# Performance work log

Measured on AMD Instinct MI355X. Metric: run time of the kernel, lower is better.

## Reference

```python
import jax, jax.numpy as jnp
import numpy as np

NUM_USER = 100000
NUM_ITEM = 50000
DIM_E = 128
DIM_FEAT = 256
BATCH = 1024
NUM_NEG = 127
TEMP = 2.0
LR_LAMBDA = 0.5
NUM_SAMPLE = 0.5


def _l2norm(x, eps=1e-12):
    n = jnp.linalg.norm(x, axis=1, keepdims=True)
    return x / jnp.maximum(n, eps)


def setup_inputs() -> dict:
    key = jax.random.key(0)
    ks = jax.random.split(key, 9)
    flat = BATCH * (1 + NUM_NEG)
    user_tensor = jax.random.randint(ks[0], (BATCH, 1 + NUM_NEG), 0, NUM_USER, dtype=jnp.int64 if jax.config.jax_enable_x64 else jnp.int32)
    item_tensor = jax.random.randint(ks[1], (BATCH, 1 + NUM_NEG), NUM_USER, NUM_USER + NUM_ITEM, dtype=user_tensor.dtype)
    rand_index = jax.random.randint(ks[2], (int(flat * NUM_SAMPLE),), 0, flat, dtype=user_tensor.dtype)
    id_embedding = jax.random.normal(ks[3], (NUM_USER + NUM_ITEM, DIM_E), jnp.float32) * 0.02
    v_feat = jax.random.normal(ks[4], (NUM_ITEM, DIM_FEAT), jnp.float32)
    W1 = jax.random.normal(ks[5], (DIM_FEAT, 256), jnp.float32) * (1.0 / np.sqrt(DIM_FEAT))
    b1 = jax.random.normal(ks[6], (256,), jnp.float32) * 0.01
    W2 = jax.random.normal(ks[7], (256, DIM_E), jnp.float32) * (1.0 / 16.0)
    b2 = jax.random.normal(ks[8], (DIM_E,), jnp.float32) * 0.01
    return {"user_tensor": user_tensor, "item_tensor": item_tensor, "rand_index": rand_index,
            "id_embedding": id_embedding, "v_feat": v_feat, "W1": W1, "b1": b1, "W2": W2, "b2": b2}


def _contrastive(anchor, all_t):
    # exp(<a,b>/T) grouped into [B, 1+num_neg]; pos is column 0
    score = jnp.exp(jnp.sum(anchor * all_t, axis=1) / TEMP).reshape(-1, 1 + NUM_NEG)
    pos = score[:, 0]
    tot = jnp.sum(score, axis=1)
    return jnp.mean(-jnp.log(pos / tot))


def reference(user_tensor, item_tensor, rand_index, id_embedding, v_feat, W1, b1, W2, b2):
    # encoder: normalize content feats, 2-layer MLP
    feature = _l2norm(v_feat)
    feature = jax.nn.leaky_relu(feature @ W1 + b1)  # slope 0.01, matches torch default
    feature = feature @ W2 + b2                      # [num_item, dim_E]

    pos_flat = jnp.repeat(item_tensor[:, 0:1], 1 + NUM_NEG, axis=1).reshape(-1)
    u_flat = user_tensor.reshape(-1)
    i_flat = item_tensor.reshape(-1)

    all_item_feat = feature[i_flat - NUM_USER]          # [flat, dim_E]
    user_emb = id_embedding[u_flat]
    pos_emb = id_embedding[pos_flat]
    all_item_emb = id_embedding[i_flat]

    head_feat = _l2norm(all_item_feat)
    head_embed = _l2norm(pos_emb)

    # replace a random half of the item embeddings with content features
    all_item_input = all_item_emb.at[rand_index].set(all_item_feat[rand_index])

    c1 = _contrastive(head_embed, head_feat)
    c2 = _contrastive(user_emb, all_item_input)

    reg_loss = (jnp.mean(jnp.sqrt(jnp.sum(user_emb ** 2, axis=1))) +
                jnp.mean(jnp.sqrt(jnp.sum(all_item_emb ** 2, axis=1)))) / 2

    # graph_generator is None -> graph contrastive loss is 0
    total = c1 * LR_LAMBDA + c2 * (1.0 - LR_LAMBDA)
    return total, reg_loss
```

## Files before the change

kernel.cpp:

```cpp
#include <hip/hip_runtime.h>
#include <math.h>

#define NUSER 100000
#define NITEM 50000
#define NID   (NUSER + NITEM)
#define DIM_E 128
#define DIM_F 256
#define BATCH 1024
#define NCOL 128
#define FLAT (BATCH * NCOL)

typedef __attribute__((ext_vector_type(8))) short bf16x8;
typedef __attribute__((ext_vector_type(4))) short bf16x4;
typedef __attribute__((ext_vector_type(4))) float f32x4;

__device__ __forceinline__ float dot4(float4 a, float4 b) {
    return a.x * b.x + a.y * b.y + a.z * b.z + a.w * b.w;
}

__device__ __forceinline__ short f2bf(float x) {
    unsigned u = __float_as_uint(x);
    unsigned r = (u + 0x7FFFu + ((u >> 16) & 1u)) >> 16;
    return (short)r;
}

__device__ __forceinline__ float bf2f(short s) {
    return __uint_as_float(((unsigned)(unsigned short)s) << 16);
}

__global__ __launch_bounds__(256) void prep0_kernel(const float* __restrict__ W1,
                                                    const float* __restrict__ W2,
                                                    short* __restrict__ w1t,
                                                    short* __restrict__ w2t,
                                                    int* __restrict__ flags) {
    int i = blockIdx.x * 256 + threadIdx.x;
    if (i < FLAT) flags[i] = 0;
    if (i < 256 * 256) {
        int n = i >> 8, k = i & 255;
        w1t[i] = f2bf(W1[(size_t)k * 256 + n]);
    } else if (i < 256 * 256 + 128 * 256) {
        int j = i - 256 * 256;
        int n = j >> 8, k = j & 255;
        w2t[j] = f2bf(W2[(size_t)k * 128 + n]);
    }
}

__device__ __forceinline__ void stage_rows(const float4 va[4], int srow, int q,
                                           short* __restrict__ As) {
    float s = 0.f;
#pragma unroll
    for (int c = 0; c < 4; ++c) s += dot4(va[c], va[c]);
#pragma unroll
    for (int off = 8; off >= 1; off >>= 1) s += __shfl_xor(s, off);
    float inv = 1.f / fmaxf(sqrtf(s), 1e-12f);
    bf16x8 p0, p1;
    p0[0] = f2bf(va[0].x * inv); p0[1] = f2bf(va[0].y * inv);
    p0[2] = f2bf(va[0].z * inv); p0[3] = f2bf(va[0].w * inv);
    p0[4] = f2bf(va[1].x * inv); p0[5] = f2bf(va[1].y * inv);
    p0[6] = f2bf(va[1].z * inv); p0[7] = f2bf(va[1].w * inv);
    p1[0] = f2bf(va[2].x * inv); p1[1] = f2bf(va[2].y * inv);
    p1[2] = f2bf(va[2].z * inv); p1[3] = f2bf(va[2].w * inv);
    p1[4] = f2bf(va[3].x * inv); p1[5] = f2bf(va[3].y * inv);
    p1[6] = f2bf(va[3].z * inv); p1[7] = f2bf(va[3].w * inv);
    const int sw = (srow & 7) << 3;
    *(bf16x8*)(&As[srow * 256 + ((q * 16) ^ sw)]) = p0;
    *(bf16x8*)(&As[srow * 256 + ((q * 16 + 8) ^ sw)]) = p1;
}

__global__ __launch_bounds__(512, 2) void fused_prep_kernel(const float* __restrict__ vfeat,
                                                            const short* __restrict__ w1t,
                                                            const float* __restrict__ b1,
                                                            const short* __restrict__ w2t,
                                                            const float* __restrict__ b2,
                                                            short* __restrict__ featout,
                                                            const float* __restrict__ idemb,
                                                            short* __restrict__ idemb_bf,
                                                            float* __restrict__ norms,
                                                            const int* __restrict__ ridx,
                                                            int nridx,
                                                            int* __restrict__ flags) {
    __shared__ __align__(16) short As[32 * 256];
    __shared__ __align__(16) short Hs[32 * 256];
    const int t = threadIdx.x;

    if (blockIdx.x >= 256) {
        const int blk = blockIdx.x - 256;
        if (blk < 128) {
            for (int i = blk * 512 + t; i < nridx; i += 128 * 512) flags[ridx[i]] = 1;
        }
        const int sub = t & 31;
        int row = blk * 16 + (t >> 5);
        for (; row < NID; row += 768 * 16) {
            float4 v = *(const float4*)(idemb + (size_t)row * DIM_E + sub * 4);
            float s = dot4(v, v);
#pragma unroll
            for (int off = 16; off >= 1; off >>= 1) s += __shfl_xor(s, off);
            bf16x4 p;
            p[0] = f2bf(v.x); p[1] = f2bf(v.y); p[2] = f2bf(v.z); p[3] = f2bf(v.w);
            *(bf16x4*)(idemb_bf + (size_t)row * DIM_E + sub * 4) = p;
            if (sub == 0) norms[row] = sqrtf(s);
        }
        return;
    }

    const int w = t >> 6;
    const int l = t & 63;
    const int fr = l & 15;
    const int kg = l >> 4;
    const int srow = t >> 4;
    const int q = t & 15;
    const int NT = (NITEM + 31) / 32;

    bf16x8 B1f[8][2];
    bf16x8 B2f[8];
#pragma unroll
    for (int kc = 0; kc < 8; ++kc) {
#pragma unroll
        for (int ct = 0; ct < 2; ++ct)
            B1f[kc][ct] = *(const bf16x8*)(w1t + (size_t)(w * 32 + ct * 16 + fr) * 256 + kc * 32 + kg * 8);
        B2f[kc] = *(const bf16x8*)(w2t + (size_t)(w * 16 + fr) * 256 + kc * 32 + kg * 8);
    }
    float b1v[2];
    b1v[0] = b1[w * 32 + fr];
    b1v[1] = b1[w * 32 + 16 + fr];
    const float b2v = b2[w * 16 + fr];

    int tile = blockIdx.x;
    {
        float4 va[4];
        int gr = tile * 32 + srow;
        const float* src = vfeat + (size_t)gr * DIM_F + q * 16;
#pragma unroll
        for (int c = 0; c < 4; ++c)
            va[c] = (gr < NITEM) ? *(const float4*)(src + c * 4) : make_float4(0.f, 0.f, 0.f, 0.f);
        stage_rows(va, srow, q, As);
    }
    __syncthreads();

    while (tile < NT) {
        const int tnext = tile + 256;
        float4 vb[4];
        if (tnext < NT) {
            int gr = tnext * 32 + srow;
            const float* src = vfeat + (size_t)gr * DIM_F + q * 16;
#pragma unroll
            for (int c = 0; c < 4; ++c)
                vb[c] = (gr < NITEM) ? *(const float4*)(src + c * 4) : make_float4(0.f, 0.f, 0.f, 0.f);
        }

        {
            f32x4 acc1[2][2];
#pragma unroll
            for (int rt = 0; rt < 2; ++rt)
#pragma unroll
                for (int ct = 0; ct < 2; ++ct) acc1[rt][ct] = (f32x4){0.f, 0.f, 0.f, 0.f};
#pragma unroll
            for (int kc = 0; kc < 8; ++kc) {
                const int kb = kc * 32 + kg * 8;
                bf16x8 af[2];
#pragma unroll
                for (int rt = 0; rt < 2; ++rt) {
                    int row = rt * 16 + fr;
                    af[rt] = *(const bf16x8*)(&As[row * 256 + (kb ^ ((row & 7) << 3))]);
                }
#pragma unroll
                for (int ct = 0; ct < 2; ++ct)
#pragma unroll
                    for (int rt = 0; rt < 2; ++rt)
                        acc1[rt][ct] = __builtin_amdgcn_mfma_f32_16x16x32_bf16(af[rt], B1f[kc][ct], acc1[rt][ct], 0, 0, 0);
            }
#pragma unroll
            for (int rt = 0; rt < 2; ++rt)
#pragma unroll
                for (int ct = 0; ct < 2; ++ct) {
                    int colH = w * 32 + ct * 16 + fr;
#pragma unroll
                    for (int r = 0; r < 4; ++r) {
                        float h = acc1[rt][ct][r] + b1v[ct];
                        h = h > 0.f ? h : 0.01f * h;
                        int row = rt * 16 + kg * 4 + r;
                        Hs[row * 256 + (colH ^ ((row & 7) << 3))] = f2bf(h);
                    }
                }
        }
        __syncthreads();

        {
            f32x4 acc2[2];
            acc2[0] = (f32x4){0.f, 0.f, 0.f, 0.f};
            acc2[1] = (f32x4){0.f, 0.f, 0.f, 0.f};
#pragma unroll
            for (int kc = 0; kc < 8; ++kc) {
                const int kb = kc * 32 + kg * 8;
#pragma unroll
                for (int rt = 0; rt < 2; ++rt) {
                    int row = rt * 16 + fr;
                    bf16x8 hf = *(const bf16x8*)(&Hs[row * 256 + (kb ^ ((row & 7) << 3))]);
                    acc2[rt] = __builtin_amdgcn_mfma_f32_16x16x32_bf16(hf, B2f[kc], acc2[rt], 0, 0, 0);
                }
            }
            const int col = w * 16 + fr;
#pragma unroll
            for (int rt = 0; rt < 2; ++rt)
#pragma unroll
                for (int r = 0; r < 4; ++r) {
                    int row = tile * 32 + rt * 16 + kg * 4 + r;
                    if (row < NITEM) featout[(size_t)row * DIM_E + col] = f2bf(acc2[rt][r] + b2v);
                }
        }

        if (tnext < NT) stage_rows(vb, srow, q, As);
        __syncthreads();
        tile = tnext;
    }
}

__global__ __launch_bounds__(128) void contrast_kernel(const int* __restrict__ user,
                                                       const int* __restrict__ item,
                                                       const int* __restrict__ flags,
                                                       const float* __restrict__ idemb,
                                                       const short* __restrict__ idemb_bf,
                                                       const float* __restrict__ norms,
                                                       const short* __restrict__ feat,
                                                       float* __restrict__ rowpart) {
    __shared__ float pe[128];
    __shared__ float s1s[64], s2s[64], rs[64];
    __shared__ float dpos[2];
    const int row = blockIdx.x >> 1;
    const int part = blockIdx.x & 1;
    const int t = threadIdx.x;

    if (t < 32) {
        int p = item[(size_t)row * NCOL];
        float4 v = *(const float4*)(idemb + (size_t)p * DIM_E + t * 4);
        float s = dot4(v, v);
#pragma unroll
        for (int off = 16; off >= 1; off >>= 1) s += __shfl_xor(s, off);
        float inv = 1.f / fmaxf(sqrtf(s), 1e-12f);
        *(float4*)(&pe[t * 4]) = make_float4(v.x * inv, v.y * inv, v.z * inv, v.w * inv);
    }
    __syncthreads();

    const int el = t >> 1;
    const int e = part * 64 + el;
    const int h = t & 1;
    const size_t j = (size_t)row * NCOL + e;
    const int u = user[j];
    const int it = item[j];
    const int fl = flags[j];
    const short* up = idemb_bf + (size_t)u * DIM_E + h * 64;
    const short* ip = idemb_bf + (size_t)it * DIM_E + h * 64;
    const short* fp = feat + (size_t)(it - NUSER) * DIM_E + h * 64;

    bf16x8 ub[8], fb[8], xb[8];
#pragma unroll
    for (int i = 0; i < 8; ++i) { ub[i] = ((const bf16x8*)up)[i]; fb[i] = ((const bf16x8*)fp)[i]; }
    if (fl) {
#pragma unroll
        for (int i = 0; i < 8; ++i) xb[i] = fb[i];
    } else {
#pragma unroll
        for (int i = 0; i < 8; ++i) xb[i] = ((const bf16x8*)ip)[i];
    }
    float nu = norms[u];
    float ni = norms[it];

    float sf = 0.f, dpf = 0.f, dux = 0.f;
#pragma unroll
    for (int i = 0; i < 8; ++i) {
        float4 p0 = *(const float4*)(&pe[h * 64 + i * 8]);
        float4 p1 = *(const float4*)(&pe[h * 64 + i * 8 + 4]);
        float pk[8] = {p0.x, p0.y, p0.z, p0.w, p1.x, p1.y, p1.z, p1.w};
#pragma unroll
        for (int k = 0; k < 8; ++k) {
            float fv = bf2f(fb[i][k]);
            float uv = bf2f(ub[i][k]);
            float xv = bf2f(xb[i][k]);
            sf += fv * fv;
            dpf += pk[k] * fv;
            dux += uv * xv;
        }
    }
    sf += __shfl_xor(sf, 1);
    dpf += __shfl_xor(dpf, 1);
    dux += __shfl_xor(dux, 1);

    if (h == 0) {
        float fnorm = fmaxf(sqrtf(sf), 1e-12f);
        float d1 = dpf / fnorm * 0.5f;
        float d2 = dux * 0.5f;
        s1s[el] = expf(d1);
        s2s[el] = expf(d2);
        rs[el] = nu + ni;
        if (e == 0) { dpos[0] = d1; dpos[1] = d2; }
    }
    __syncthreads();

    if (t < 32) {
        float a1 = s1s[t] + s1s[t + 32];
        float a2 = s2s[t] + s2s[t + 32];
        float a3 = rs[t] + rs[t + 32];
#pragma unroll
        for (int off = 16; off >= 1; off >>= 1) {
            a1 += __shfl_xor(a1, off);
            a2 += __shfl_xor(a2, off);
            a3 += __shfl_xor(a3, off);
        }
        if (t == 0) {
            float* dst = rowpart + (size_t)blockIdx.x * 6;
            dst[0] = a1;
            dst[1] = a2;
            dst[2] = a3;
            if (part == 0) { dst[3] = dpos[0]; dst[4] = dpos[1]; }
        }
    }
}

__global__ __launch_bounds__(256) void finalize_kernel(const float* __restrict__ rowpart,
                                                       float* __restrict__ out) {
    float c1 = 0.f, c2 = 0.f, rg = 0.f;
    for (int r = threadIdx.x; r < BATCH; r += 256) {
        const float* p0 = rowpart + (size_t)(r * 2) * 6;
        const float* p1 = rowpart + (size_t)(r * 2 + 1) * 6;
        float A1 = p0[0] + p1[0];
        float A2 = p0[1] + p1[1];
        c1 += logf(A1) - p0[3];
        c2 += logf(A2) - p0[4];
        rg += p0[2] + p1[2];
    }
#pragma unroll
    for (int off = 32; off >= 1; off >>= 1) {
        c1 += __shfl_xor(c1, off);
        c2 += __shfl_xor(c2, off);
        rg += __shfl_xor(rg, off);
    }
    __shared__ float buf[4][3];
    int wid = threadIdx.x >> 6, lane = threadIdx.x & 63;
    if (lane == 0) { buf[wid][0] = c1; buf[wid][1] = c2; buf[wid][2] = rg; }
    __syncthreads();
    if (threadIdx.x == 0) {
        float C1 = buf[0][0] + buf[1][0] + buf[2][0] + buf[3][0];
        float C2 = buf[0][1] + buf[1][1] + buf[2][1] + buf[3][1];
        float R  = buf[0][2] + buf[1][2] + buf[2][2] + buf[3][2];
        out[0] = 0.5f * (C1 / (float)BATCH) + 0.5f * (C2 / (float)BATCH);
        out[1] = 0.5f * (R / (float)FLAT);
    }
}

extern "C" void kernel_launch(void* const* d_in, const int* in_sizes, int n_in,
                              void* d_out, int out_size, void* d_ws, size_t ws_size,
                              hipStream_t stream) {
    const int* user = (const int*)d_in[0];
    const int* item = (const int*)d_in[1];
    const int* ridx = (const int*)d_in[2];
    const float* idemb = (const float*)d_in[3];
    const float* vfeat = (const float*)d_in[4];
    const float* W1 = (const float*)d_in[5];
    const float* b1 = (const float*)d_in[6];
    const float* W2 = (const float*)d_in[7];
    const float* b2 = (const float*)d_in[8];
    float* out = (float*)d_out;

    char* ws = (char*)d_ws;
    short* feat_bf  = (short*)(ws);
    short* idemb_bf = (short*)(ws + 12800000);
    float* norms    = (float*)(ws + 51200000);
    int*   flags    = (int*)  (ws + 51800000);
    float* rowpart  = (float*)(ws + 52324288);
    short* w1t      = (short*)(ws + 52373440);
    short* w2t      = (short*)(ws + 52504512);

    const int nridx = in_sizes[2];

    prep0_kernel<<<dim3(512), dim3(256), 0, stream>>>(W1, W2, w1t, w2t, flags);
    fused_prep_kernel<<<dim3(1024), dim3(512), 0, stream>>>(vfeat, w1t, b1, w2t, b2, feat_bf,
                                                            idemb, idemb_bf, norms,
                                                            ridx, nridx, flags);
    contrast_kernel<<<dim3(2 * BATCH), dim3(128), 0, stream>>>(user, item, flags, idemb,
                                                               idemb_bf, norms, feat_bf, rowpart);
    finalize_kernel<<<dim3(1), dim3(256), 0, stream>>>(rowpart, out);
}
```

Before: 77.97 us.

## Warp-specialize fused prep kernel so extra waves convert embeddings alongside MLP

Before, the prep kernel ran 1024 blocks: 256 MLP blocks and 768 blocks that converted the id embedding to bf16 and computed row norms. Now it runs 256 blocks of 768 threads. In each block, 8 waves run the MLP tiles while 4 extra waves do the embedding conversion and the flag scatter, interleaved between the block barriers. The goal is to overlap the memory-bound conversion with the MFMA work inside the same blocks. The contrast kernel also builds the normalized positive embedding from the precomputed norms and the bf16 copy instead of re-reading fp32 rows. The cost is lower occupancy (one block per CU). Only 4 waves per block now handle the 150k-row sweep, so the sweep may take longer than the MLP and stall it at the barriers.

```diff
diff --git a/kernel.cpp b/kernel.cpp
--- a/kernel.cpp
+++ b/kernel.cpp
@@ -9,6 +9,8 @@
 #define BATCH 1024
 #define NCOL 128
 #define FLAT (BATCH * NCOL)
+#define NT   ((NITEM + 31) / 32)
+#define SWEEPS ((NID + 2047) / 2048)
 
 typedef __attribute__((ext_vector_type(8))) short bf16x8;
 typedef __attribute__((ext_vector_type(4))) short bf16x4;
@@ -67,41 +69,24 @@
     *(bf16x8*)(&As[srow * 256 + ((q * 16 + 8) ^ sw)]) = p1;
 }
 
-__global__ __launch_bounds__(512, 2) void fused_prep_kernel(const float* __restrict__ vfeat,
-                                                            const short* __restrict__ w1t,
-                                                            const float* __restrict__ b1,
-                                                            const short* __restrict__ w2t,
-                                                            const float* __restrict__ b2,
-                                                            short* __restrict__ featout,
-                                                            const float* __restrict__ idemb,
-                                                            short* __restrict__ idemb_bf,
-                                                            float* __restrict__ norms,
-                                                            const int* __restrict__ ridx,
-                                                            int nridx,
-                                                            int* __restrict__ flags) {
+__global__ __launch_bounds__(768, 1) void fused_kernel(const float* __restrict__ vfeat,
+                                                       const short* __restrict__ w1t,
+                                                       const float* __restrict__ b1,
+                                                       const short* __restrict__ w2t,
+                                                       const float* __restrict__ b2,
+                                                       short* __restrict__ featout,
+                                                       const float* __restrict__ idemb,
+                                                       short* __restrict__ idemb_bf,
+                                                       float* __restrict__ norms,
+                                                       const int* __restrict__ ridx,
+                                                       int nridx,
+                                                       int* __restrict__ flags) {
     __shared__ __align__(16) short As[32 * 256];
     __shared__ __align__(16) short Hs[32 * 256];
     const int t = threadIdx.x;
-
-    if (blockIdx.x >= 256) {
-        const int blk = blockIdx.x - 256;
-        if (blk < 128) {
-            for (int i = blk * 512 + t; i < nridx; i += 128 * 512) flags[ridx[i]] = 1;
-        }
-        const int sub = t & 31;
-        int row = blk * 16 + (t >> 5);
-        for (; row < NID; row += 768 * 16) {
-            float4 v = *(const float4*)(idemb + (size_t)row * DIM_E + sub * 4);
-            float s = dot4(v, v);
-#pragma unroll
-            for (int off = 16; off >= 1; off >>= 1) s += __shfl_xor(s, off);
-            bf16x4 p;
-            p[0] = f2bf(v.x); p[1] = f2bf(v.y); p[2] = f2bf(v.z); p[3] = f2bf(v.w);
-            *(bf16x4*)(idemb_bf + (size_t)row * DIM_E + sub * 4) = p;
-            if (sub == 0) norms[row] = sqrtf(s);
-        }
-        return;
-    }
+    const int b = blockIdx.x;
+    const int nt = (NT - b + 255) / 256;
+    const int ct = t - 512;
 
     const int w = t >> 6;
     const int l = t & 63;
@@ -109,51 +94,56 @@
     const int kg = l >> 4;
     const int srow = t >> 4;
     const int q = t & 15;
-    const int NT = (NITEM + 31) / 32;
 
     bf16x8 B1f[8][2];
     bf16x8 B2f[8];
-#pragma unroll
-    for (int kc = 0; kc < 8; ++kc) {
-#pragma unroll
-        for (int ct = 0; ct < 2; ++ct)
-            B1f[kc][ct] = *(const bf16x8*)(w1t + (size_t)(w * 32 + ct * 16 + fr) * 256 + kc * 32 + kg * 8);
-        B2f[kc] = *(const bf16x8*)(w2t + (size_t)(w * 16 + fr) * 256 + kc * 32 + kg * 8);
-    }
     float b1v[2];
-    b1v[0] = b1[w * 32 + fr];
-    b1v[1] = b1[w * 32 + 16 + fr];
-    const float b2v = b2[w * 16 + fr];
-
-    int tile = blockIdx.x;
-    {
+    float b2v = 0.f;
+    if (t < 512) {
+#pragma unroll
+        for (int kc = 0; kc < 8; ++kc) {
+#pragma unroll
+            for (int ct2 = 0; ct2 < 2; ++ct2)
+                B1f[kc][ct2] = *(const bf16x8*)(w1t + (size_t)(w * 32 + ct2 * 16 + fr) * 256 + kc * 32 + kg * 8);
+            B2f[kc] = *(const bf16x8*)(w2t + (size_t)(w * 16 + fr) * 256 + kc * 32 + kg * 8);
+        }
+        b1v[0] = b1[w * 32 + fr];
+        b1v[1] = b1[w * 32 + 16 + fr];
+        b2v = b2[w * 16 + fr];
+
         float4 va[4];
-        int gr = tile * 32 + srow;
+        int gr = b * 32 + srow;
         const float* src = vfeat + (size_t)gr * DIM_F + q * 16;
 #pragma unroll
         for (int c = 0; c < 4; ++c)
             va[c] = (gr < NITEM) ? *(const float4*)(src + c * 4) : make_float4(0.f, 0.f, 0.f, 0.f);
         stage_rows(va, srow, q, As);
+    } else {
+        for (int i = b * 256 + ct; i < nridx; i += 256 * 256) flags[ridx[i]] = 1;
     }
     __syncthreads();
 
-    while (tile < NT) {
+    int sweep = 0;
+    const int K = (SWEEPS + 2 * nt - 1) / (2 * nt);
+
+    for (int it = 0; it < nt; ++it) {
+        const int tile = b + it * 256;
         const int tnext = tile + 256;
         float4 vb[4];
-        if (tnext < NT) {
-            int gr = tnext * 32 + srow;
-            const float* src = vfeat + (size_t)gr * DIM_F + q * 16;
-#pragma unroll
-            for (int c = 0; c < 4; ++c)
-                vb[c] = (gr < NITEM) ? *(const float4*)(src + c * 4) : make_float4(0.f, 0.f, 0.f, 0.f);
-        }
-
-        {
+
+        if (t < 512) {
+            if (tnext < NT) {
+                int gr = tnext * 32 + srow;
+                const float* src = vfeat + (size_t)gr * DIM_F + q * 16;
+#pragma unroll
+                for (int c = 0; c < 4; ++c)
+                    vb[c] = (gr < NITEM) ? *(const float4*)(src + c * 4) : make_float4(0.f, 0.f, 0.f, 0.f);
+            }
             f32x4 acc1[2][2];
 #pragma unroll
             for (int rt = 0; rt < 2; ++rt)
 #pragma unroll
-                for (int ct = 0; ct < 2; ++ct) acc1[rt][ct] = (f32x4){0.f, 0.f, 0.f, 0.f};
+                for (int c2 = 0; c2 < 2; ++c2) acc1[rt][c2] = (f32x4){0.f, 0.f, 0.f, 0.f};
 #pragma unroll
             for (int kc = 0; kc < 8; ++kc) {
                 const int kb = kc * 32 + kg * 8;
@@ -164,28 +154,43 @@
                     af[rt] = *(const bf16x8*)(&As[row * 256 + (kb ^ ((row & 7) << 3))]);
                 }
 #pragma unroll
-                for (int ct = 0; ct < 2; ++ct)
+                for (int c2 = 0; c2 < 2; ++c2)
 #pragma unroll
                     for (int rt = 0; rt < 2; ++rt)
-                        acc1[rt][ct] = __builtin_amdgcn_mfma_f32_16x16x32_bf16(af[rt], B1f[kc][ct], acc1[rt][ct], 0, 0, 0);
+                        acc1[rt][c2] = __builtin_amdgcn_mfma_f32_16x16x32_bf16(af[rt], B1f[kc][c2], acc1[rt][c2], 0, 0, 0);
             }
 #pragma unroll
             for (int rt = 0; rt < 2; ++rt)
 #pragma unroll
-                for (int ct = 0; ct < 2; ++ct) {
-                    int colH = w * 32 + ct * 16 + fr;
+                for (int c2 = 0; c2 < 2; ++c2) {
+                    int colH = w * 32 + c2 * 16 + fr;
 #pragma unroll
                     for (int r = 0; r < 4; ++r) {
-                        float h = acc1[rt][ct][r] + b1v[ct];
+                        float h = acc1[rt][c2][r] + b1v[c2];
                         h = h > 0.f ? h : 0.01f * h;
                         int row = rt * 16 + kg * 4 + r;
                         Hs[row * 256 + (colH ^ ((row & 7) << 3))] = f2bf(h);
                     }
                 }
+        } else {
+            for (int k2 = 0; k2 < K && sweep < SWEEPS; ++k2, ++sweep) {
+                int row = b * 8 + (ct >> 5) + sweep * 2048;
+                if (row < NID) {
+                    int sub = ct & 31;
+                    float4 v = *(const float4*)(idemb + (size_t)row * DIM_E + sub * 4);
+                    float s = dot4(v, v);
+#pragma unroll
+                    for (int off = 16; off >= 1; off >>= 1) s += __shfl_xor(s, off);
+                    bf16x4 p;
+                    p[0] = f2bf(v.x); p[1] = f2bf(v.y); p[2] = f2bf(v.z); p[3] = f2bf(v.w);
+                    *(bf16x4*)(idemb_bf + (size_t)row * DIM_E + sub * 4) = p;
+                    if (sub == 0) norms[row] = sqrtf(s);
+                }
+            }
         }
         __syncthreads();
 
-        {
+        if (t < 512) {
             f32x4 acc2[2];
             acc2[0] = (f32x4){0.f, 0.f, 0.f, 0.f};
             acc2[1] = (f32x4){0.f, 0.f, 0.f, 0.f};
@@ -207,18 +212,30 @@
                     int row = tile * 32 + rt * 16 + kg * 4 + r;
                     if (row < NITEM) featout[(size_t)row * DIM_E + col] = f2bf(acc2[rt][r] + b2v);
                 }
-        }
-
-        if (tnext < NT) stage_rows(vb, srow, q, As);
+            if (tnext < NT) stage_rows(vb, srow, q, As);
+        } else {
+            for (int k2 = 0; k2 < K && sweep < SWEEPS; ++k2, ++sweep) {
+                int row = b * 8 + (ct >> 5) + sweep * 2048;
+                if (row < NID) {
+                    int sub = ct & 31;
+                    float4 v = *(const float4*)(idemb + (size_t)row * DIM_E + sub * 4);
+                    float s = dot4(v, v);
+#pragma unroll
+                    for (int off = 16; off >= 1; off >>= 1) s += __shfl_xor(s, off);
+                    bf16x4 p;
+                    p[0] = f2bf(v.x); p[1] = f2bf(v.y); p[2] = f2bf(v.z); p[3] = f2bf(v.w);
+                    *(bf16x4*)(idemb_bf + (size_t)row * DIM_E + sub * 4) = p;
+                    if (sub == 0) norms[row] = sqrtf(s);
+                }
+            }
+        }
         __syncthreads();
-        tile = tnext;
     }
 }
 
 __global__ __launch_bounds__(128) void contrast_kernel(const int* __restrict__ user,
                                                        const int* __restrict__ item,
                                                        const int* __restrict__ flags,
-                                                       const float* __restrict__ idemb,
                                                        const short* __restrict__ idemb_bf,
                                                        const float* __restrict__ norms,
                                                        const short* __restrict__ feat,
@@ -232,12 +249,12 @@
 
     if (t < 32) {
         int p = item[(size_t)row * NCOL];
-        float4 v = *(const float4*)(idemb + (size_t)p * DIM_E + t * 4);
-        float s = dot4(v, v);
-#pragma unroll
-        for (int off = 16; off >= 1; off >>= 1) s += __shfl_xor(s, off);
-        float inv = 1.f / fmaxf(sqrtf(s), 1e-12f);
-        *(float4*)(&pe[t * 4]) = make_float4(v.x * inv, v.y * inv, v.z * inv, v.w * inv);
+        float inv = 1.f / fmaxf(norms[p], 1e-12f);
+        bf16x4 v = *(const bf16x4*)(idemb_bf + (size_t)p * DIM_E + t * 4);
+        pe[t * 4 + 0] = bf2f(v[0]) * inv;
+        pe[t * 4 + 1] = bf2f(v[1]) * inv;
+        pe[t * 4 + 2] = bf2f(v[2]) * inv;
+        pe[t * 4 + 3] = bf2f(v[3]) * inv;
     }
     __syncthreads();
 
@@ -373,10 +390,9 @@
     const int nridx = in_sizes[2];
 
     prep0_kernel<<<dim3(512), dim3(256), 0, stream>>>(W1, W2, w1t, w2t, flags);
-    fused_prep_kernel<<<dim3(1024), dim3(512), 0, stream>>>(vfeat, w1t, b1, w2t, b2, feat_bf,
-                                                            idemb, idemb_bf, norms,
-                                                            ridx, nridx, flags);
-    contrast_kernel<<<dim3(2 * BATCH), dim3(128), 0, stream>>>(user, item, flags, idemb,
+    fused_kernel<<<dim3(256), dim3(768), 0, stream>>>(vfeat, w1t, b1, w2t, b2, feat_bf,
+                                                      idemb, idemb_bf, norms, ridx, nridx, flags);
+    contrast_kernel<<<dim3(2 * BATCH), dim3(128), 0, stream>>>(user, item, flags,
                                                                idemb_bf, norms, feat_bf, rowpart);
     finalize_kernel<<<dim3(1), dim3(256), 0, stream>>>(rowpart, out);
 }
```

Result: slower. 109.1 us (+39.9%).
